# Kernel tuning notes

Hardware: AMD Instinct MI355X
Metric: run time of the kernel (lower is better)

## Reference

```python
import jax, jax.numpy as jnp
import numpy as np

BINS = 10
MOMENTUM = 0.75  # first-call acc_sum = (1 - MOMENTUM) * num_in_bin (acc_sum starts at 0)
BS, CLA = 1048576, 32


def _smooth(bins):
    s = 1.0 - 25.0 * (np.arange(bins, dtype=np.float64) / bins) ** 2
    s[int(bins * 0.2):] = 0.0
    s[s < 0] = 0.0
    return jnp.asarray(s, jnp.float32)


def setup_inputs() -> dict:
    key = jax.random.key(0)
    k1, k2, k3 = jax.random.split(key, 3)
    targets = jax.random.bernoulli(k1, 0.5, (BS, CLA)).astype(jnp.float32)
    # per-row noise scale so g = mean|inputs-targets| spreads over the low bins (<0.3)
    row_scale = jax.random.uniform(k3, (BS, 1), minval=0.01, maxval=0.3)
    noise = jax.random.uniform(k2, (BS, CLA)) * row_scale
    inputs = jnp.clip(jnp.abs(targets - noise), 1e-4, 1.0 - 1e-4)
    return {"inputs": inputs, "targets": targets}


def reference(inputs, targets):
    bins, m = BINS, MOMENTUM
    bs, cla = inputs.shape
    tot = float(bs * cla)
    # g uses inputs.detach(); binning/weighting is non-differentiable anyway
    g = jax.lax.stop_gradient(jnp.mean(jnp.abs(inputs - targets), axis=1))  # [bs]
    # edges are i/bins (last edge 1+1e-6): bin index = floor(g*bins), clipped
    idx = jnp.clip(jnp.floor(g * bins).astype(jnp.int32), 0, bins - 1)
    counts = jnp.zeros((bins,), jnp.float32).at[idx].add(1.0)  # histogram
    acc_sum = (1.0 - m) * counts  # momentum update from acc_sum=0
    smooth = _smooth(bins)
    safe_acc = jnp.where(acc_sum > 0, acc_sum, 1.0)
    per_bin_w = jnp.where(counts > 0, smooth * tot / safe_acc, 0.0)  # [bins]
    w = per_bin_w[idx]  # [bs]
    w = w * w
    w = w / jnp.sum(w)
    w = jnp.where(w < 1e-6, 0.0, w)
    # elementwise BCE on probabilities, mean over classes, weighted sum over batch
    loss_el = -(targets * jnp.log(inputs) + (1.0 - targets) * jnp.log1p(-inputs))
    return jnp.sum(jnp.mean(loss_el, axis=1) * w)
```

## Files before the change

### kernel.cpp

```cpp
#include <hip/hip_runtime.h>

#define BS_ROWS 1048576
#define CLA 32
#define NBINS 10
#define GRID 2048
#define RPB 32
#define BATCH 4
#define OUTER 4

__global__ __launch_bounds__(256) void ghm_pass1(
    const float* __restrict__ in, const float* __restrict__ tg,
    float* __restrict__ cnt, float* __restrict__ bsum)
{
    __shared__ float s_cnt[NBINS];
    __shared__ float s_bsum[NBINS];
    const int tid = threadIdx.x;
    if (tid < NBINS) { s_cnt[tid] = 0.0f; s_bsum[tid] = 0.0f; }
    __syncthreads();

    const unsigned sub = tid & 7;
    const unsigned rg  = tid >> 3;
    const unsigned row0 = blockIdx.x * RPB + rg;
    const unsigned sstride = GRID * RPB;

    #pragma unroll 1
    for (int outer = 0; outer < OUTER; ++outer) {
        const unsigned rbase = row0 + (unsigned)outer * (sstride * BATCH);

        float4 iv[BATCH], tv[BATCH];
        #pragma unroll
        for (int j = 0; j < BATCH; ++j) {
            const unsigned off = (rbase + j * sstride) * CLA + sub * 4;
            iv[j] = *(const float4*)(in + off);
            tv[j] = *(const float4*)(tg + off);
        }

        float gs[BATCH], bs[BATCH];
        #pragma unroll
        for (int j = 0; j < BATCH; ++j) {
            gs[j] = fabsf(iv[j].x - tv[j].x) + fabsf(iv[j].y - tv[j].y)
                  + fabsf(iv[j].z - tv[j].z) + fabsf(iv[j].w - tv[j].w);
            float a0 = tv[j].x > 0.5f ? iv[j].x : 1.0f - iv[j].x;
            float a1 = tv[j].y > 0.5f ? iv[j].y : 1.0f - iv[j].y;
            float a2 = tv[j].z > 0.5f ? iv[j].z : 1.0f - iv[j].z;
            float a3 = tv[j].w > 0.5f ? iv[j].w : 1.0f - iv[j].w;
            bs[j] = -(__logf(a0) + __logf(a1) + __logf(a2) + __logf(a3));
        }

        #pragma unroll
        for (int off = 1; off < 8; off <<= 1) {
            #pragma unroll
            for (int j = 0; j < BATCH; ++j) {
                gs[j] += __shfl_xor(gs[j], off);
                bs[j] += __shfl_xor(bs[j], off);
            }
        }

        if (sub == 0) {
            #pragma unroll
            for (int j = 0; j < BATCH; ++j) {
                float g = gs[j] * (1.0f / 32.0f);
                int idx = (int)floorf(g * 10.0f);
                idx = idx < 0 ? 0 : (idx > NBINS - 1 ? NBINS - 1 : idx);
                atomicAdd(&s_cnt[idx], 1.0f);
                atomicAdd(&s_bsum[idx], bs[j] * (1.0f / 32.0f));
            }
        }
    }
    __syncthreads();
    if (tid < NBINS) {
        atomicAdd(&cnt[tid], s_cnt[tid]);
        atomicAdd(&bsum[tid], s_bsum[tid]);
    }
}

__global__ void ghm_pass2(const float* __restrict__ cnt,
                          const float* __restrict__ bsum,
                          float* __restrict__ out)
{
    if (threadIdx.x == 0 && blockIdx.x == 0) {
        const double tot = (double)BS_ROWS * (double)CLA;
        const float smooth[NBINS] = {1.0f, 0.75f, 0,0,0,0,0,0,0,0};
        double pbw2[NBINS];
        double sum_w = 0.0;
        for (int b = 0; b < NBINS; ++b) {
            double c = (double)cnt[b];
            double pbw = (c > 0.0 && smooth[b] > 0.0f)
                       ? (double)smooth[b] * tot / (0.25 * c) : 0.0;
            pbw2[b] = pbw * pbw;
            sum_w += c * pbw2[b];
        }
        double loss = 0.0;
        for (int b = 0; b < NBINS; ++b) {
            double w = (sum_w > 0.0) ? pbw2[b] / sum_w : 0.0;
            if (w < 1e-6) w = 0.0;
            loss += (double)bsum[b] * w;
        }
        out[0] = (float)loss;
    }
}

extern "C" void kernel_launch(void* const* d_in, const int* in_sizes, int n_in,
                              void* d_out, int out_size, void* d_ws, size_t ws_size,
                              hipStream_t stream) {
    const float* in = (const float*)d_in[0];
    const float* tg = (const float*)d_in[1];
    float* ws   = (float*)d_ws;
    float* cnt  = ws;
    float* bsum = ws + NBINS;

    hipMemsetAsync(d_ws, 0, 2 * NBINS * sizeof(float), stream);

    ghm_pass1<<<GRID, 256, 0, stream>>>(in, tg, cnt, bsum);
    ghm_pass2<<<1, 64, 0, stream>>>(cnt, bsum, (float*)d_out);
}
```

Before: 83.65 us.

## Use contiguous per-block row chunks with LDS transpose reduction instead of shuffles

Each block now processes a contiguous 512-row chunk, loading fully coalesced float4 streams, and writes per-segment partial sums to padded shared memory. One thread per row then reduces its 8 partials and does the histogram atomics, replacing the xor-shuffle tree and the sub==0-only atomics. Logs are computed with log2 times ln2. The change adds two block barriers per round and LDS traffic, and it removes the floor before the int cast, which is equivalent only because g is non-negative.

Result: no change. 82.12 us (-1.8%).

```diff
diff --git a/kernel.cpp b/kernel.cpp
--- a/kernel.cpp
+++ b/kernel.cpp
@@ -4,70 +4,73 @@
 #define CLA 32
 #define NBINS 10
 #define GRID 2048
-#define RPB 32
-#define BATCH 4
-#define OUTER 4
+#define RPB 512
+#define RROWS 256
+#define NROUNDS 2
+#define LN2 0.69314718055994531f
 
 __global__ __launch_bounds__(256) void ghm_pass1(
     const float* __restrict__ in, const float* __restrict__ tg,
     float* __restrict__ cnt, float* __restrict__ bsum)
 {
+    __shared__ float gpart[RROWS][9];
+    __shared__ float bpart[RROWS][9];
     __shared__ float s_cnt[NBINS];
     __shared__ float s_bsum[NBINS];
+
     const int tid = threadIdx.x;
     if (tid < NBINS) { s_cnt[tid] = 0.0f; s_bsum[tid] = 0.0f; }
-    __syncthreads();
 
-    const unsigned sub = tid & 7;
-    const unsigned rg  = tid >> 3;
-    const unsigned row0 = blockIdx.x * RPB + rg;
-    const unsigned sstride = GRID * RPB;
+    const float4* __restrict__ in4 = (const float4*)in;
+    const float4* __restrict__ tg4 = (const float4*)tg;
+    const unsigned blk4 = blockIdx.x * (RPB * CLA / 4);
 
-    #pragma unroll 1
-    for (int outer = 0; outer < OUTER; ++outer) {
-        const unsigned rbase = row0 + (unsigned)outer * (sstride * BATCH);
-
-        float4 iv[BATCH], tv[BATCH];
-        #pragma unroll
-        for (int j = 0; j < BATCH; ++j) {
-            const unsigned off = (rbase + j * sstride) * CLA + sub * 4;
-            iv[j] = *(const float4*)(in + off);
-            tv[j] = *(const float4*)(tg + off);
-        }
-
-        float gs[BATCH], bs[BATCH];
-        #pragma unroll
-        for (int j = 0; j < BATCH; ++j) {
-            gs[j] = fabsf(iv[j].x - tv[j].x) + fabsf(iv[j].y - tv[j].y)
-                  + fabsf(iv[j].z - tv[j].z) + fabsf(iv[j].w - tv[j].w);
-            float a0 = tv[j].x > 0.5f ? iv[j].x : 1.0f - iv[j].x;
-            float a1 = tv[j].y > 0.5f ? iv[j].y : 1.0f - iv[j].y;
-            float a2 = tv[j].z > 0.5f ? iv[j].z : 1.0f - iv[j].z;
-            float a3 = tv[j].w > 0.5f ? iv[j].w : 1.0f - iv[j].w;
-            bs[j] = -(__logf(a0) + __logf(a1) + __logf(a2) + __logf(a3));
-        }
+    #pragma unroll
+    for (int r = 0; r < NROUNDS; ++r) {
+        const unsigned base4 = blk4 + r * (RROWS * CLA / 4);
 
         #pragma unroll
-        for (int off = 1; off < 8; off <<= 1) {
+        for (int gq = 0; gq < 2; ++gq) {
+            float4 iv[4], tv[4];
             #pragma unroll
-            for (int j = 0; j < BATCH; ++j) {
-                gs[j] += __shfl_xor(gs[j], off);
-                bs[j] += __shfl_xor(bs[j], off);
+            for (int j = 0; j < 4; ++j) {
+                const unsigned fi = base4 + (unsigned)(gq * 4 + j) * 256u + tid;
+                iv[j] = in4[fi];
+                tv[j] = tg4[fi];
+            }
+            #pragma unroll
+            for (int j = 0; j < 4; ++j) {
+                const unsigned idx = (unsigned)(gq * 4 + j) * 256u + tid;
+                const unsigned row = idx >> 3, seg = idx & 7;
+
+                float gp = fabsf(iv[j].x - tv[j].x) + fabsf(iv[j].y - tv[j].y)
+                         + fabsf(iv[j].z - tv[j].z) + fabsf(iv[j].w - tv[j].w);
+                float a0 = tv[j].x > 0.5f ? iv[j].x : 1.0f - iv[j].x;
+                float a1 = tv[j].y > 0.5f ? iv[j].y : 1.0f - iv[j].y;
+                float a2 = tv[j].z > 0.5f ? iv[j].z : 1.0f - iv[j].z;
+                float a3 = tv[j].w > 0.5f ? iv[j].w : 1.0f - iv[j].w;
+                float bp = -LN2 * (__log2f(a0) + __log2f(a1)
+                                 + __log2f(a2) + __log2f(a3));
+
+                gpart[row][seg] = gp;
+                bpart[row][seg] = bp;
             }
         }
+        __syncthreads();
 
-        if (sub == 0) {
+        {
+            float g = 0.0f, b = 0.0f;
             #pragma unroll
-            for (int j = 0; j < BATCH; ++j) {
-                float g = gs[j] * (1.0f / 32.0f);
-                int idx = (int)floorf(g * 10.0f);
-                idx = idx < 0 ? 0 : (idx > NBINS - 1 ? NBINS - 1 : idx);
-                atomicAdd(&s_cnt[idx], 1.0f);
-                atomicAdd(&s_bsum[idx], bs[j] * (1.0f / 32.0f));
-            }
+            for (int k = 0; k < 8; ++k) { g += gpart[tid][k]; b += bpart[tid][k]; }
+            g *= (1.0f / 32.0f);
+            int bi = (int)(g * 10.0f);
+            bi = bi < 0 ? 0 : (bi > NBINS - 1 ? NBINS - 1 : bi);
+            atomicAdd(&s_cnt[bi], 1.0f);
+            atomicAdd(&s_bsum[bi], b * (1.0f / 32.0f));
         }
+        __syncthreads();
     }
-    __syncthreads();
+
     if (tid < NBINS) {
         atomicAdd(&cnt[tid], s_cnt[tid]);
         atomicAdd(&bsum[tid], s_bsum[tid]);
```

## Use contiguous per-block row tiles, DPP lane reductions, and larger load batches

Applied to the files above, without the earlier changes.

Each block now reads a contiguous 512-row chunk instead of rows strided across the whole grid. Loads are issued in batches of 8 float4 pairs per thread over 2 outer iterations. The 8-lane shuffle reductions are replaced with DPP adds (quad xor1, xor2, row half-mirror) so the cross-lane sums avoid LDS-based shuffles. The launch bounds now request 4 waves per SIMD, which risks register pressure from the larger batch. Bin indexing drops floorf for a truncating cast, which is equivalent for non-negative g.

Result: faster. 80.71 us (-3.5%).

```diff
diff --git a/kernel.cpp b/kernel.cpp
--- a/kernel.cpp
+++ b/kernel.cpp
@@ -4,11 +4,20 @@
 #define CLA 32
 #define NBINS 10
 #define GRID 2048
-#define RPB 32
-#define BATCH 4
-#define OUTER 4
+#define RPB 512
+#define BATCH 8
+#define OUTER 2
 
-__global__ __launch_bounds__(256) void ghm_pass1(
+template <int CTRL>
+__device__ __forceinline__ float dpp_add(float v) {
+    int x = __builtin_amdgcn_update_dpp(0, __float_as_int(v), CTRL, 0xF, 0xF, true);
+    return v + __int_as_float(x);
+}
+#define DPP_XOR1 0xB1
+#define DPP_XOR2 0x4E
+#define DPP_HMIR 0x141
+
+__global__ __launch_bounds__(256, 4) void ghm_pass1(
     const float* __restrict__ in, const float* __restrict__ tg,
     float* __restrict__ cnt, float* __restrict__ bsum)
 {
@@ -20,53 +29,50 @@
 
     const unsigned sub = tid & 7;
     const unsigned rg  = tid >> 3;
-    const unsigned row0 = blockIdx.x * RPB + rg;
-    const unsigned sstride = GRID * RPB;
+    const float4* __restrict__ in4 = (const float4*)in;
+    const float4* __restrict__ tg4 = (const float4*)tg;
+    const unsigned base = blockIdx.x * (RPB * CLA / 4);
 
     #pragma unroll 1
     for (int outer = 0; outer < OUTER; ++outer) {
-        const unsigned rbase = row0 + (unsigned)outer * (sstride * BATCH);
-
         float4 iv[BATCH], tv[BATCH];
         #pragma unroll
         for (int j = 0; j < BATCH; ++j) {
-            const unsigned off = (rbase + j * sstride) * CLA + sub * 4;
-            iv[j] = *(const float4*)(in + off);
-            tv[j] = *(const float4*)(tg + off);
+            const unsigned fi = base + (unsigned)(outer * BATCH + j) * 256u
+                              + rg * 8u + sub;
+            iv[j] = in4[fi];
+            tv[j] = tg4[fi];
         }
 
-        float gs[BATCH], bs[BATCH];
+        float garr[BATCH], barr[BATCH];
         #pragma unroll
         for (int j = 0; j < BATCH; ++j) {
-            gs[j] = fabsf(iv[j].x - tv[j].x) + fabsf(iv[j].y - tv[j].y)
-                  + fabsf(iv[j].z - tv[j].z) + fabsf(iv[j].w - tv[j].w);
+            float gp = fabsf(iv[j].x - tv[j].x) + fabsf(iv[j].y - tv[j].y)
+                     + fabsf(iv[j].z - tv[j].z) + fabsf(iv[j].w - tv[j].w);
             float a0 = tv[j].x > 0.5f ? iv[j].x : 1.0f - iv[j].x;
             float a1 = tv[j].y > 0.5f ? iv[j].y : 1.0f - iv[j].y;
             float a2 = tv[j].z > 0.5f ? iv[j].z : 1.0f - iv[j].z;
             float a3 = tv[j].w > 0.5f ? iv[j].w : 1.0f - iv[j].w;
-            bs[j] = -(__logf(a0) + __logf(a1) + __logf(a2) + __logf(a3));
-        }
+            float bp = -(__logf(a0) + __logf(a1) + __logf(a2) + __logf(a3));
 
-        #pragma unroll
-        for (int off = 1; off < 8; off <<= 1) {
-            #pragma unroll
-            for (int j = 0; j < BATCH; ++j) {
-                gs[j] += __shfl_xor(gs[j], off);
-                bs[j] += __shfl_xor(bs[j], off);
-            }
+            gp = dpp_add<DPP_XOR1>(gp);  bp = dpp_add<DPP_XOR1>(bp);
+            gp = dpp_add<DPP_XOR2>(gp);  bp = dpp_add<DPP_XOR2>(bp);
+            gp = dpp_add<DPP_HMIR>(gp);  bp = dpp_add<DPP_HMIR>(bp);
+            garr[j] = gp;  barr[j] = bp;
         }
 
         if (sub == 0) {
             #pragma unroll
             for (int j = 0; j < BATCH; ++j) {
-                float g = gs[j] * (1.0f / 32.0f);
-                int idx = (int)floorf(g * 10.0f);
-                idx = idx < 0 ? 0 : (idx > NBINS - 1 ? NBINS - 1 : idx);
-                atomicAdd(&s_cnt[idx], 1.0f);
-                atomicAdd(&s_bsum[idx], bs[j] * (1.0f / 32.0f));
+                float g = garr[j] * (1.0f / 32.0f);
+                int bi = (int)(g * 10.0f);
+                bi = bi < 0 ? 0 : (bi > NBINS - 1 ? NBINS - 1 : bi);
+                atomicAdd(&s_cnt[bi], 1.0f);
+                atomicAdd(&s_bsum[bi], barr[j] * (1.0f / 32.0f));
             }
         }
     }
+
     __syncthreads();
     if (tid < NBINS) {
         atomicAdd(&cnt[tid], s_cnt[tid]);
@@ -109,7 +115,7 @@
     float* cnt  = ws;
     float* bsum = ws + NBINS;
 
-    hipMemsetAsync(d_ws, 0, 2 * NBINS * sizeof(float), stream);
+    (void)hipMemsetAsync(d_ws, 0, 2 * NBINS * sizeof(float), stream);
 
     ghm_pass1<<<GRID, 256, 0, stream>>>(in, tg, cnt, bsum);
     ghm_pass2<<<1, 64, 0, stream>>>(cnt, bsum, (float*)d_out);
```
